# Optimization experiments

Measured on AMD Instinct MI355X. Metric: run time of the kernel, lower is better.

Reference implementation:

```python
import jax, jax.numpy as jnp
import numpy as np

H, D, LORA = 12, 64, 64  # n_heads, headdim, decay-LoRA rank


def _time_mix(x, mu, w_bias, dw1, dw2, u, Wr, Wk, Wv, Wg, Wo, ln_w, ln_b):
    """RWKV-6 time-mix (single direction). x: (B,T,C)."""
    B, T, C = x.shape
    # token shift: previous token (zero-padded at t=0)
    xs = jnp.concatenate([jnp.zeros_like(x[:, :1]), x[:, :-1]], axis=1)
    dx = xs - x
    xr, xk, xv, xw, xg = (x + dx * mu[i] for i in range(5))  # order: r,k,v,w,g
    r = (xr @ Wr).reshape(B, T, H, D)
    k = (xk @ Wk).reshape(B, T, H, D)
    v = (xv @ Wv).reshape(B, T, H, D)
    g = jax.nn.silu(xg @ Wg)                                   # (B,T,C)
    # data-dependent per-channel decay in (0,1)
    w = jnp.exp(-jnp.exp(w_bias + jnp.tanh(xw @ dw1) @ dw2)).reshape(B, T, H, D)

    def step(S, rkvw):  # S: (B,H,D,D) state
        r_t, k_t, v_t, w_t = rkvw          # each (B,H,D)
        kv = k_t[..., None] * v_t[:, :, None, :]               # (B,H,D,D)
        y_t = jnp.einsum('bhd,bhde->bhe', r_t, S + u[None, :, :, None] * kv)
        return w_t[..., None] * S + kv, y_t

    seq = tuple(jnp.moveaxis(a, 1, 0) for a in (r, k, v, w))   # (T,B,H,D)
    S0 = jnp.zeros((B, H, D, D), x.dtype)
    _, ys = jax.lax.scan(step, S0, seq)
    y = jnp.moveaxis(ys, 0, 1)                                 # (B,T,H,D)
    # per-head GroupNorm (n_heads groups over d_model)
    mean = y.mean(-1, keepdims=True)
    var = y.var(-1, keepdims=True)
    y = ((y - mean) * jax.lax.rsqrt(var + 1e-5)).reshape(B, T, C) * ln_w + ln_b
    return (y * g) @ Wo


def reference(x, pad_mask, mu, w_bias, dw1, dw2, u, Wr, Wk, Wv, Wg, Wo, ln_w, ln_b):
    p = lambda i: (mu[i], w_bias[i], dw1[i], dw2[i], u[i], Wr[i], Wk[i], Wv[i],
                   Wg[i], Wo[i], ln_w[i], ln_b[i])
    fwd_out = _time_mix(x, *p(0))
    bwd_out = _time_mix(x[:, ::-1], *p(1))[:, ::-1]
    out = fwd_out + bwd_out
    out = out * pad_mask[..., None].astype(out.dtype)
    return out


def setup_inputs() -> dict:
    key = jax.random.key(0)
    ks = jax.random.split(key, 12)
    B, T, C = 4, 1024, 768
    s = C ** -0.5
    return {
        'x': jax.random.normal(ks[0], (B, T, C), jnp.float32),
        'pad_mask': jnp.ones((B, T), jnp.bool_),
        'mu': jax.random.uniform(ks[1], (2, 5, C), jnp.float32),
        'w_bias': jax.random.normal(ks[2], (2, C), jnp.float32) * 0.3 - 0.5,
        'dw1': jax.random.normal(ks[3], (2, C, LORA), jnp.float32) * s,
        'dw2': jax.random.normal(ks[4], (2, LORA, C), jnp.float32) * 0.1,
        'u': jax.random.normal(ks[5], (2, H, D), jnp.float32) * 0.5,
        'Wr': jax.random.normal(ks[6], (2, C, C), jnp.float32) * s,
        'Wk': jax.random.normal(ks[7], (2, C, C), jnp.float32) * s,
        'Wv': jax.random.normal(ks[8], (2, C, C), jnp.float32) * s,
        'Wg': jax.random.normal(ks[9], (2, C, C), jnp.float32) * s,
        'Wo': jax.random.normal(ks[10], (2, C, C), jnp.float32) * s,
        'ln_w': jnp.ones((2, C), jnp.float32),
        'ln_b': jnp.zeros((2, C), jnp.float32),
    }
```

## Files before the change

kernel.cpp:

```cpp
#include <hip/hip_runtime.h>
#include <cstdint>
#include <cstddef>


#define HH   12
#define DD   64
#define CC   768
#define TT   1024
#define BBB  4
#define LR   64
#define BT   (BBB*TT)
#define WSQ  (CC*CC)

typedef unsigned short u16;
typedef _Float16 f16x8 __attribute__((ext_vector_type(8)));
typedef float f32x4 __attribute__((ext_vector_type(4)));

__device__ __forceinline__ u16 f2h(float f) {
    const _Float16 h = (_Float16)f;
    return __builtin_bit_cast(u16, h);
}
__device__ __forceinline__ float h2f(u16 h) {
    return (float)__builtin_bit_cast(_Float16, h);
}

__device__ __forceinline__ void gl_lds16(const void* g, void* l) {
    __builtin_amdgcn_global_load_lds(
        (const __attribute__((address_space(1))) void*)g,
        (__attribute__((address_space(3))) void*)l, 16, 0, 0);
}

__device__ __forceinline__ float mask_val(const void* mp, int idx) {
    const unsigned char* b = (const unsigned char*)mp;
    const int i0 = ((const int*)mp)[0];
    if (i0 == 0x3f800000) {
        return ((const float*)mp)[idx] != 0.f ? 1.f : 0.f;
    }
    if ((b[1] | b[2] | b[3]) == 0) {
        return ((const int*)mp)[idx] != 0 ? 1.f : 0.f;
    }
    return b[idx] ? 1.f : 0.f;
}

struct TP10 { const float* src[10]; };

__global__ __launch_bounds__(256)
void transpose_conv(TP10 tj, u16* __restrict__ dst)
{
    __shared__ float sh[32][33];
    const int j = blockIdx.z;
    const float* __restrict__ src = tj.src[j];
    u16* __restrict__ d = dst + (size_t)j * WSQ;
    const int n0 = blockIdx.x << 5, k0 = blockIdx.y << 5;
    const int tx = threadIdx.x & 31, ty = threadIdx.x >> 5;
    #pragma unroll
    for (int i = 0; i < 4; ++i)
        sh[ty + (i << 3)][tx] = src[(size_t)(k0 + ty + (i << 3)) * CC + n0 + tx];
    __syncthreads();
    #pragma unroll
    for (int i = 0; i < 4; ++i)
        d[(size_t)(n0 + ty + (i << 3)) * CC + k0 + tx] =
            f2h(sh[tx][ty + (i << 3)]);
}

__global__ __launch_bounds__(256)
void convert_x(const float* __restrict__ x, u16* __restrict__ xb)
{
    const size_t off = ((size_t)blockIdx.x * 256 + threadIdx.x) * 8;
    const float4 a = *reinterpret_cast<const float4*>(x + off);
    const float4 b = *reinterpret_cast<const float4*>(x + off + 4);
    uint4 w;
    w.x = (unsigned)f2h(a.x) | ((unsigned)f2h(a.y) << 16);
    w.y = (unsigned)f2h(a.z) | ((unsigned)f2h(a.w) << 16);
    w.z = (unsigned)f2h(b.x) | ((unsigned)f2h(b.y) << 16);
    w.w = (unsigned)f2h(b.z) | ((unsigned)f2h(b.w) << 16);
    *reinterpret_cast<uint4*>(xb + off) = w;
}

__global__ __launch_bounds__(256)
void convert_mu(const float* __restrict__ mu, u16* __restrict__ muh, int n)
{
    const int i = blockIdx.x * 256 + threadIdx.x;
    if (i < n) muh[i] = f2h(mu[i]);
}

__global__ __launch_bounds__(256)
void mix4_kernel(const u16* __restrict__ xb, const u16* __restrict__ muh,
                 u16* __restrict__ mx, const int dbase)
{
    const int j = blockIdx.y;
    const int slot = blockIdx.z;
    const int dir = dbase + slot;
    const int idx = blockIdx.x * 256 + threadIdx.x;
    const int s = idx / 96;
    const int c = (idx - s * 96) << 3;
    const int b = s >> 10, ts = s & (TT - 1);
    const int t = dir ? (TT - 1 - ts) : ts;
    const int tp = dir ? (t + 1) : (t - 1);
    const int musel = (j == 3) ? 4 : j;

    const uint4 xa4 = *reinterpret_cast<const uint4*>(
        xb + (size_t)(b * TT + t) * CC + c);
    uint4 xp4 = make_uint4(0u, 0u, 0u, 0u);
    if (ts > 0)
        xp4 = *reinterpret_cast<const uint4*>(
            xb + (size_t)(b * TT + tp) * CC + c);
    const uint4 m4 = *reinterpret_cast<const uint4*>(
        muh + (size_t)dir * 5 * CC + musel * CC + c);

    const f16x8 xa = __builtin_bit_cast(f16x8, xa4);
    const f16x8 xp = __builtin_bit_cast(f16x8, xp4);
    const f16x8 mm = __builtin_bit_cast(f16x8, m4);
    const f16x8 res = (xp - xa) * mm + xa;

    u16* __restrict__ dst = mx + (size_t)((slot << 2) + j) * ((size_t)BT * CC);
    *reinterpret_cast<uint4*>(dst + (size_t)s * CC + c) =
        __builtin_bit_cast(uint4, res);
}

struct GB { const u16* Wt[8]; const u16* Ab[8]; float* out[8];
            const float* mu[8]; int act[8]; int dirv[8]; };

__global__ __launch_bounds__(256)
void gemm_mfma_big(GB p, const u16* __restrict__ xb,
                   const int K, const int N, const int mixA)
{
    const int j = blockIdx.z;
    const u16* __restrict__ Wt = p.Wt[j];
    const u16* __restrict__ Ab = p.Ab[j];
    float* __restrict__ out = p.out[j];
    const float* __restrict__ mu = p.mu[j];
    const int act = p.act[j];
    const int dir = p.dirv[j];

    __shared__ __align__(16) u16 Als[128][64];
    __shared__ __align__(16) u16 Bls[128][64];
    const int tid = threadIdx.x;
    const int rowbase = blockIdx.x << 7;
    const int colbase = blockIdx.y << 7;
    const int lane = tid & 63;
    const int wid = tid >> 6;
    const int wr = (wid >> 1) << 6;
    const int wc = (wid & 1) << 6;
    const int lm = lane & 15;

    const int lrow = lane >> 3;
    const int gcol = (((lane & 7) ^ lrow) << 3);

    f32x4 acc[4][4] = {};

    for (int k0 = 0; k0 < K; k0 += 64) {
        if (mixA) {
            #pragma unroll
            for (int it = 0; it < 4; ++it) {
                const int c   = tid + (it << 8);
                const int row = c >> 3;
                const int ch  = c & 7;
                const int kq  = (ch ^ (row & 7)) << 3;
                *reinterpret_cast<uint4*>(&Bls[row][ch << 3]) =
                    *reinterpret_cast<const uint4*>(
                        Wt + (size_t)(colbase + row) * K + k0 + kq);
                const int s  = rowbase + row;
                const int bb = s >> 10, ts = s & (TT - 1);
                const int t  = dir ? (TT - 1 - ts) : ts;
                const int tp = dir ? (t + 1) : (t - 1);
                const uint4 xa4 = *reinterpret_cast<const uint4*>(
                    xb + (size_t)(bb * TT + t) * CC + k0 + kq);
                uint4 xp4 = make_uint4(0u, 0u, 0u, 0u);
                if (ts > 0)
                    xp4 = *reinterpret_cast<const uint4*>(
                        xb + (size_t)(bb * TT + tp) * CC + k0 + kq);
                const u16* as = reinterpret_cast<const u16*>(&xa4);
                const u16* ps = reinterpret_cast<const u16*>(&xp4);
                const float4 m0 = *reinterpret_cast<const float4*>(mu + k0 + kq);
                const float4 m1 = *reinterpret_cast<const float4*>(mu + k0 + kq + 4);
                const float mm[8] = {m0.x, m0.y, m0.z, m0.w,
                                     m1.x, m1.y, m1.z, m1.w};
                uint4 w;
                unsigned rr[4];
                #pragma unroll
                for (int q = 0; q < 4; ++q) {
                    const float a0 = h2f(as[2 * q]);
                    const float a1 = h2f(as[2 * q + 1]);
                    const float p0 = h2f(ps[2 * q]);
                    const float p1 = h2f(ps[2 * q + 1]);
                    const float v0 = fmaf(p0 - a0, mm[2 * q], a0);
                    const float v1 = fmaf(p1 - a1, mm[2 * q + 1], a1);
                    rr[q] = (unsigned)f2h(v0) | ((unsigned)f2h(v1) << 16);
                }
                w.x = rr[0]; w.y = rr[1]; w.z = rr[2]; w.w = rr[3];
                *reinterpret_cast<uint4*>(&Als[row][ch << 3]) = w;
            }
        } else {
            #pragma unroll
            for (int i = 0; i < 4; ++i) {
                const int rb  = (wid << 5) + (i << 3);
                const int row = rb + lrow;
                gl_lds16(Ab + (size_t)(rowbase + row) * K + k0 + gcol,
                         &Als[rb][0]);
                gl_lds16(Wt + (size_t)(colbase + row) * K + k0 + gcol,
                         &Bls[rb][0]);
            }
        }
        __syncthreads();
        #pragma unroll
        for (int ks = 0; ks < 2; ++ks) {
            const int gc = (ks << 2) + (lane >> 4);
            const int sl = (gc ^ (lm & 7)) << 3;
            f16x8 av[4], bv[4];
            #pragma unroll
            for (int mi = 0; mi < 4; ++mi)
                av[mi] = *reinterpret_cast<const f16x8*>(
                    &Als[wr + mi * 16 + lm][sl]);
            #pragma unroll
            for (int ni = 0; ni < 4; ++ni)
                bv[ni] = *reinterpret_cast<const f16x8*>(
                    &Bls[wc + ni * 16 + lm][sl]);
            #pragma unroll
            for (int mi = 0; mi < 4; ++mi)
                #pragma unroll
                for (int ni = 0; ni < 4; ++ni)
                    acc[mi][ni] = __builtin_amdgcn_mfma_f32_16x16x32_f16(
                        av[mi], bv[ni], acc[mi][ni], 0, 0, 0);
        }
        __syncthreads();
    }

    #pragma unroll
    for (int mi = 0; mi < 4; ++mi) {
        #pragma unroll
        for (int r = 0; r < 4; ++r) {
            const int srow = rowbase + wr + mi * 16 + ((lane >> 4) << 2) + r;
            if (act <= 1) {
                #pragma unroll
                for (int ni = 0; ni < 4; ++ni) {
                    float v = acc[mi][ni][r];
                    if (act == 1) v = v / (1.f + expf(-v));
                    out[(size_t)srow * N + colbase + wc + ni * 16 + lm] = v;
                }
            } else {
                const int b2  = srow >> 10;
                const int ts2 = srow & (TT - 1);
                const int t2  = dir ? (TT - 1 - ts2) : ts2;
                float* op = out + (size_t)(b2 * TT + t2) * CC + colbase + wc + lm;
                #pragma unroll
                for (int ni = 0; ni < 4; ++ni)
                    op[ni * 16] = acc[mi][ni][r];
            }
        }
    }
}

__global__ __launch_bounds__(256)
void combine_kernel(float* __restrict__ out, const float* __restrict__ obuf,
                    const void* __restrict__ mask)
{
    const size_t idx = ((size_t)blockIdx.x * 256 + threadIdx.x) * 4;
    const int row = (int)(idx / CC);
    const float mv = mask_val(mask, row);
    const float4 a = *reinterpret_cast<const float4*>(out + idx);
    const float4 b = *reinterpret_cast<const float4*>(obuf + idx);
    *reinterpret_cast<float4*>(out + idx) = make_float4(
        (a.x + b.x) * mv, (a.y + b.y) * mv, (a.z + b.z) * mv, (a.w + b.w) * mv);
}

__global__ __launch_bounds__(256)
void lora1_kernel(const float* __restrict__ x, const float* __restrict__ mu,
                  const float* __restrict__ dw1, float* __restrict__ out,
                  const int dbase)
{
    __shared__ float As[16][68];
    __shared__ float Bs[64][68];
    const int tid = threadIdx.x;
    const int rowbase = blockIdx.x << 4;
    const int slot = blockIdx.y;
    const int dir = dbase + slot;
    const float* __restrict__ muD = mu + (size_t)dir * 5 * CC + 3 * CC;
    const float* __restrict__ dw1p = dw1 + (size_t)dir * CC * LR;
    float* __restrict__ outp = out + (size_t)slot * BT * LR;

    const int arow = tid >> 4;
    const int akq  = (tid & 15) << 2;
    const int s  = rowbase + arow;
    const int bb = s >> 10, ts = s & (TT - 1);
    const int t  = dir ? (TT - 1 - ts) : ts;
    const int tp = dir ? (t + 1) : (t - 1);

    const int c0 = tid & 63;
    const int r4 = tid >> 6;

    float acc[4] = {0.f, 0.f, 0.f, 0.f};

    for (int k0 = 0; k0 < CC; k0 += 64) {
        {
            const int c = k0 + akq;
            const float4 xa = *reinterpret_cast<const float4*>(
                x + (size_t)(bb * TT + t) * CC + c);
            float4 xp = make_float4(0.f, 0.f, 0.f, 0.f);
            if (ts > 0)
                xp = *reinterpret_cast<const float4*>(
                    x + (size_t)(bb * TT + tp) * CC + c);
            const float4 m4 = *reinterpret_cast<const float4*>(muD + c);
            float4 va;
            va.x = fmaf(xp.x - xa.x, m4.x, xa.x);
            va.y = fmaf(xp.y - xa.y, m4.y, xa.y);
            va.z = fmaf(xp.z - xa.z, m4.z, xa.z);
            va.w = fmaf(xp.w - xa.w, m4.w, xa.w);
            *reinterpret_cast<float4*>(&As[arow][akq]) = va;
        }
        #pragma unroll
        for (int it = 0; it < 4; ++it) {
            const int c2 = tid + (it << 8);
            const int brow = c2 >> 4, bcol = (c2 & 15) << 2;
            *reinterpret_cast<float4*>(&Bs[brow][bcol]) =
                *reinterpret_cast<const float4*>(
                    dw1p + (size_t)(k0 + brow) * LR + bcol);
        }
        __syncthreads();
        #pragma unroll
        for (int k4 = 0; k4 < 16; ++k4) {
            float bv[4];
            #pragma unroll
            for (int q = 0; q < 4; ++q) bv[q] = Bs[(k4 << 2) + q][c0];
            #pragma unroll
            for (int i = 0; i < 4; ++i) {
                const float4 a4 = *reinterpret_cast<const float4*>(
                    &As[r4 + (i << 2)][k4 << 2]);
                acc[i] = fmaf(a4.x, bv[0], acc[i]);
                acc[i] = fmaf(a4.y, bv[1], acc[i]);
                acc[i] = fmaf(a4.z, bv[2], acc[i]);
                acc[i] = fmaf(a4.w, bv[3], acc[i]);
            }
        }
        __syncthreads();
    }
    #pragma unroll
    for (int i = 0; i < 4; ++i)
        outp[(size_t)(rowbase + r4 + (i << 2)) * LR + c0] = tanhf(acc[i]);
}

__global__ __launch_bounds__(256)
void gemm_kernel(const float* __restrict__ lora, const float* __restrict__ dw2,
                 const float* __restrict__ wbias, float* __restrict__ wwbuf,
                 const int dbase)
{
    __shared__ float As[16][68];
    __shared__ float Bs[16][68];
    const int tid = threadIdx.x;
    const int rowbase = blockIdx.x << 6;
    const int colbase = blockIdx.y << 6;
    const int slot = blockIdx.z;
    const int dir = dbase + slot;
    const float* __restrict__ Ap = lora + (size_t)slot * BT * LR;
    const float* __restrict__ W  = dw2 + (size_t)dir * LR * CC;
    const float* __restrict__ bias = wbias + (size_t)dir * CC;
    float* __restrict__ out = wwbuf + (size_t)slot * BT * CC;

    const int ty = tid >> 4, tx = tid & 15;
    const int am = tid >> 2;
    const int aq = tid & 3;
    const int s  = rowbase + am;
    const int bk = tid >> 4;
    const int bn = (tid & 15) << 2;

    float acc[4][4];
    #pragma unroll
    for (int i = 0; i < 4; ++i)
        #pragma unroll
        for (int j = 0; j < 4; ++j) acc[i][j] = 0.f;

    for (int k0 = 0; k0 < LR; k0 += 16) {
        const float4 va = *reinterpret_cast<const float4*>(
            Ap + (size_t)s * LR + k0 + (aq << 2));
        const float4 vb = *reinterpret_cast<const float4*>(
            W + (size_t)(k0 + bk) * CC + colbase + bn);
        As[(aq << 2) + 0][am] = va.x;
        As[(aq << 2) + 1][am] = va.y;
        As[(aq << 2) + 2][am] = va.z;
        As[(aq << 2) + 3][am] = va.w;
        *reinterpret_cast<float4*>(&Bs[bk][bn]) = vb;
        __syncthreads();
        #pragma unroll
        for (int kk = 0; kk < 16; ++kk) {
            const float4 a  = *reinterpret_cast<const float4*>(&As[kk][ty << 2]);
            const float4 bv = *reinterpret_cast<const float4*>(&Bs[kk][tx << 2]);
            const float av[4]  = {a.x, a.y, a.z, a.w};
            const float bvv[4] = {bv.x, bv.y, bv.z, bv.w};
            #pragma unroll
            for (int i = 0; i < 4; ++i)
                #pragma unroll
                for (int j = 0; j < 4; ++j)
                    acc[i][j] = fmaf(av[i], bvv[j], acc[i][j]);
        }
        __syncthreads();
    }

    #pragma unroll
    for (int i = 0; i < 4; ++i) {
        const int srow = rowbase + (ty << 2) + i;
        const int ncol = colbase + (tx << 2);
        float v[4];
        #pragma unroll
        for (int j = 0; j < 4; ++j)
            v[j] = expf(-expf(acc[i][j] + bias[ncol + j]));
        *reinterpret_cast<float4*>(out + (size_t)srow * CC + ncol) =
            make_float4(v[0], v[1], v[2], v[3]);
    }
}

template<int L>
__global__ __launch_bounds__(64)
void scanA_kernel(const float* __restrict__ kbuf, const float* __restrict__ vbuf,
                  const float* __restrict__ wbuf,
                  float* __restrict__ SL, float* __restrict__ Pbuf)
{
    constexpr int NCHL = TT / L;
    constexpr size_t SLN = (size_t)NCHL * BBB * HH * DD * DD;
    constexpr size_t PN  = (size_t)NCHL * BBB * HH * DD;
    __shared__ float lk[L * DD], lw[L * DD], lv[L * DD];
    const int c = blockIdx.x, h = blockIdx.y;
    const int b = blockIdx.z & (BBB - 1);
    const int slot = blockIdx.z >> 2;
    const size_t boff = (size_t)slot * BT * CC;
    const int e = threadIdx.x;
    const int rowq = e >> 4;
    const int col  = (e & 15) << 2;

    const size_t gbase = boff + (size_t)(b * TT + c * L) * CC + h * DD;
    #pragma unroll
    for (int r4 = 0; r4 < L / 4; ++r4) {
        const int row = (r4 << 2) + rowq;
        const size_t ga = gbase + (size_t)row * CC + col;
        *reinterpret_cast<float4*>(&lk[row * DD + col]) =
            *reinterpret_cast<const float4*>(kbuf + ga);
        *reinterpret_cast<float4*>(&lw[row * DD + col]) =
            *reinterpret_cast<const float4*>(wbuf + ga);
        *reinterpret_cast<float4*>(&lv[row * DD + col]) =
            *reinterpret_cast<const float4*>(vbuf + ga);
    }
    __syncthreads();

    float S[DD];
    #pragma unroll
    for (int d = 0; d < DD; ++d) S[d] = 0.f;
    float P = 1.f;

    for (int t = 0; t < L; ++t) {
        const float ve = lv[t * DD + e];
        P *= lw[t * DD + e];
        #pragma unroll
        for (int d4 = 0; d4 < 16; ++d4) {
            const float4 k4 = *reinterpret_cast<const float4*>(&lk[t * DD + (d4 << 2)]);
            const float4 w4 = *reinterpret_cast<const float4*>(&lw[t * DD + (d4 << 2)]);
            S[(d4 << 2) + 0] = fmaf(w4.x, S[(d4 << 2) + 0], k4.x * ve);
            S[(d4 << 2) + 1] = fmaf(w4.y, S[(d4 << 2) + 1], k4.y * ve);
            S[(d4 << 2) + 2] = fmaf(w4.z, S[(d4 << 2) + 2], k4.z * ve);
            S[(d4 << 2) + 3] = fmaf(w4.w, S[(d4 << 2) + 3], k4.w * ve);
        }
    }

    float* slotp = SL + (size_t)slot * SLN
                 + (size_t)((c * BBB + b) * HH + h) * DD * DD;
    #pragma unroll
    for (int d = 0; d < DD; ++d) slotp[d * DD + e] = S[d];
    Pbuf[(size_t)slot * PN + (size_t)((c * BBB + b) * HH + h) * DD + e] = P;
}

__global__ __launch_bounds__(64)
void scanB_kernel(float* __restrict__ SL, const float* __restrict__ Pbuf,
                  const int nch)
{
    const int h = blockIdx.x, b = blockIdx.y;
    const int dg = blockIdx.z & 3;
    const int slot = blockIdx.z >> 2;
    const size_t SLN = (size_t)nch * BBB * HH * DD * DD;
    const size_t PN  = (size_t)nch * BBB * HH * DD;
    float* __restrict__ SLs = SL + (size_t)slot * SLN;
    const float* __restrict__ Ps = Pbuf + (size_t)slot * PN;
    const int e = threadIdx.x;
    const size_t doff = (size_t)dg * 16 * DD;

    float S[16];
    #pragma unroll
    for (int i = 0; i < 16; ++i) S[i] = 0.f;

    float sl[16], pp[16];
    {
        const float* s0 = SLs + (size_t)(b * HH + h) * DD * DD + doff;
        const float* p0 = Ps + (size_t)(b * HH + h) * DD + dg * 16;
        #pragma unroll
        for (int i = 0; i < 16; ++i) { sl[i] = s0[i * DD + e]; pp[i] = p0[i]; }
    }
    for (int c = 0; c < nch; ++c) {
        float sl2[16], pp2[16];
        if (c + 1 < nch) {
            const float* s1 = SLs + (size_t)(((c + 1) * BBB + b) * HH + h) * DD * DD + doff;
            const float* p1 = Ps + (size_t)(((c + 1) * BBB + b) * HH + h) * DD + dg * 16;
            #pragma unroll
            for (int i = 0; i < 16; ++i) { sl2[i] = s1[i * DD + e]; pp2[i] = p1[i]; }
        }
        float* sc = SLs + (size_t)((c * BBB + b) * HH + h) * DD * DD + doff;
        #pragma unroll
        for (int i = 0; i < 16; ++i) {
            S[i] = fmaf(pp[i], S[i], sl[i]);
            sc[i * DD + e] = S[i];
        }
        #pragma unroll
        for (int i = 0; i < 16; ++i) { sl[i] = sl2[i]; pp[i] = pp2[i]; }
    }
}

template<int L>
__global__ __launch_bounds__(64)
void scanC_kernel(const float* __restrict__ rbuf, const float* __restrict__ kbuf,
                  const float* __restrict__ vbuf, const float* __restrict__ wbuf,
                  const float* __restrict__ gbuf, const float* __restrict__ SL,
                  const float* __restrict__ u, const float* __restrict__ lnw,
                  const float* __restrict__ lnb, u16* __restrict__ zb,
                  const int dbase)
{
    constexpr int NCHL = TT / L;
    constexpr size_t SLN = (size_t)NCHL * BBB * HH * DD * DD;
    __shared__ float lr[L * DD], lk[L * DD], lw[L * DD];
    const int c = blockIdx.x, h = blockIdx.y;
    const int b = blockIdx.z & (BBB - 1);
    const int slot = blockIdx.z >> 2;
    const int dir = dbase + slot;
    const size_t boff = (size_t)slot * BT * CC;
    const int e = threadIdx.x;
    const int rowq = e >> 4;
    const int col  = (e & 15) << 2;

    const size_t gbase = boff + (size_t)(b * TT + c * L) * CC + h * DD;
    #pragma unroll
    for (int r4 = 0; r4 < L / 4; ++r4) {
        const int row = (r4 << 2) + rowq;
        const size_t ga = gbase + (size_t)row * CC + col;
        *reinterpret_cast<float4*>(&lr[row * DD + col]) =
            *reinterpret_cast<const float4*>(rbuf + ga);
        *reinterpret_cast<float4*>(&lk[row * DD + col]) =
            *reinterpret_cast<const float4*>(kbuf + ga);
        *reinterpret_cast<float4*>(&lw[row * DD + col]) =
            *reinterpret_cast<const float4*>(wbuf + ga);
    }
    __syncthreads();

    const float ue = u[(size_t)(dir * HH + h) * DD + e];
    const float gw = lnw[dir * CC + h * DD + e];
    const float gb = lnb[dir * CC + h * DD + e];

    float S[DD];
    if (c == 0) {
        #pragma unroll
        for (int d = 0; d < DD; ++d) S[d] = 0.f;
    } else {
        const float* slotp = SL + (size_t)slot * SLN
                           + (size_t)(((c - 1) * BBB + b) * HH + h) * DD * DD;
        #pragma unroll
        for (int d = 0; d < DD; ++d) S[d] = slotp[d * DD + e];
    }

    float ve = vbuf[gbase + e];
    float ge = gbuf[gbase + e];
    for (int t = 0; t < L; ++t) {
        float ve2 = 0.f, ge2 = 0.f;
        if (t + 1 < L) {
            ve2 = vbuf[gbase + (size_t)(t + 1) * CC + e];
            ge2 = gbuf[gbase + (size_t)(t + 1) * CC + e];
        }
        float coef = lr[t * DD + e] * ue * lk[t * DD + e];
        #pragma unroll
        for (int off = 32; off > 0; off >>= 1) coef += __shfl_xor(coef, off);

        float y0 = 0.f, y1 = 0.f, y2 = 0.f, y3 = 0.f;
        #pragma unroll
        for (int d4 = 0; d4 < 16; ++d4) {
            const float4 r4 = *reinterpret_cast<const float4*>(&lr[t * DD + (d4 << 2)]);
            const float4 k4 = *reinterpret_cast<const float4*>(&lk[t * DD + (d4 << 2)]);
            const float4 w4 = *reinterpret_cast<const float4*>(&lw[t * DD + (d4 << 2)]);
            y0 = fmaf(r4.x, S[(d4 << 2) + 0], y0);
            y1 = fmaf(r4.y, S[(d4 << 2) + 1], y1);
            y2 = fmaf(r4.z, S[(d4 << 2) + 2], y2);
            y3 = fmaf(r4.w, S[(d4 << 2) + 3], y3);
            S[(d4 << 2) + 0] = fmaf(w4.x, S[(d4 << 2) + 0], k4.x * ve);
            S[(d4 << 2) + 1] = fmaf(w4.y, S[(d4 << 2) + 1], k4.y * ve);
            S[(d4 << 2) + 2] = fmaf(w4.z, S[(d4 << 2) + 2], k4.z * ve);
            S[(d4 << 2) + 3] = fmaf(w4.w, S[(d4 << 2) + 3], k4.w * ve);
        }
        float y = ((y0 + y1) + (y2 + y3)) + coef * ve;

        float sum = y, sq = y * y;
        #pragma unroll
        for (int off = 32; off > 0; off >>= 1) {
            sum += __shfl_xor(sum, off);
            sq  += __shfl_xor(sq, off);
        }
        const float mean = sum * (1.f / 64.f);
        const float var  = fmaf(-mean, mean, sq * (1.f / 64.f));
        const float yn   = (y - mean) * rsqrtf(var + 1e-5f) * gw + gb;
        zb[gbase + (size_t)t * CC + e] = f2h(yn * ge);
        ve = ve2;
        ge = ge2;
    }
}

extern "C" void kernel_launch(void* const* d_in, const int* in_sizes, int n_in,
                              void* d_out, int out_size, void* d_ws, size_t ws_size,
                              hipStream_t stream)
{
    const float* x     = (const float*)d_in[0];
    const void*  mask  = d_in[1];
    const float* mu    = (const float*)d_in[2];
    const float* wbias = (const float*)d_in[3];
    const float* dw1   = (const float*)d_in[4];
    const float* dw2   = (const float*)d_in[5];
    const float* u     = (const float*)d_in[6];
    const float* Wr    = (const float*)d_in[7];
    const float* Wk    = (const float*)d_in[8];
    const float* Wv    = (const float*)d_in[9];
    const float* Wg    = (const float*)d_in[10];
    const float* Wo    = (const float*)d_in[11];
    const float* lnw   = (const float*)d_in[12];
    const float* lnb   = (const float*)d_in[13];
    float* out = (float*)d_out;

    float* ws = (float*)d_ws;
    const size_t NBT = (size_t)BT * CC;
    const size_t MUN = 2 * 5 * CC;

    auto fits = [&](int nd, int nch, bool mb) -> bool {
        const size_t SLN = (size_t)nch * BBB * HH * DD * DD;
        const size_t PN  = (size_t)nch * BBB * HH * DD;
        const size_t fl = (size_t)nd * (5 * NBT + (size_t)BT * LR + SLN + PN);
        const size_t hw = (size_t)(nd + 1) * NBT + (size_t)10 * WSQ + MUN
                        + (mb ? (size_t)4 * nd * NBT : 0);
        return fl * 4 + hw * 2 <= ws_size;
    };
    int nd, nch; bool mixbuf;
    if      (fits(2, 64, true)) { nd = 2; nch = 64; mixbuf = true; }
    else if (fits(2, 32, true)) { nd = 2; nch = 32; mixbuf = true; }
    else if (fits(2, 16, true)) { nd = 2; nch = 16; mixbuf = true; }
    else {
        nd = 1;
        mixbuf = fits(1, 16, true);
        nch = fits(1, 64, mixbuf) ? 64 : fits(1, 32, mixbuf) ? 32 : 16;
    }
    const size_t SLN = (size_t)nch * BBB * HH * DD * DD;
    const size_t PN  = (size_t)nch * BBB * HH * DD;

    float* rbuf  = ws;
    float* kbuf  = rbuf  + (size_t)nd * NBT;
    float* vbuf  = kbuf  + (size_t)nd * NBT;
    float* wwbuf = vbuf  + (size_t)nd * NBT;
    float* gbuf  = wwbuf + (size_t)nd * NBT;
    float* lora  = gbuf  + (size_t)nd * NBT;
    float* SL    = lora  + (size_t)nd * BT * LR;
    float* Pbuf  = SL    + (size_t)nd * SLN;
    u16*   zb    = (u16*)(Pbuf + (size_t)nd * PN);
    u16*   xbb   = zb + (size_t)nd * NBT;
    u16*   wtb   = xbb + NBT;
    u16*   muh   = wtb + (size_t)10 * WSQ;
    u16*   mx    = muh + MUN;
    float* obuf  = rbuf;

    TP10 tj;
    const float* Wlist[5] = {Wr, Wk, Wv, Wg, Wo};
    for (int dir = 0; dir < 2; ++dir)
        for (int i = 0; i < 5; ++i)
            tj.src[dir * 5 + i] = Wlist[i] + (size_t)dir * WSQ;
    transpose_conv<<<dim3(24, 24, 10), 256, 0, stream>>>(tj, wtb);
    convert_x<<<dim3((int)(NBT / (8 * 256))), 256, 0, stream>>>(x, xbb);
    convert_mu<<<dim3((int)((MUN + 255) / 256)), 256, 0, stream>>>(mu, muh, (int)MUN);

    auto launch_scans = [&](int ndl, int dbase) {
        const dim3 zA(TT / (TT / nch), 1, 1);
        if (nch == 64) {
            scanA_kernel<16><<<dim3(64, HH, BBB * ndl), dim3(64), 0, stream>>>(
                kbuf, vbuf, wwbuf, SL, Pbuf);
            scanB_kernel<<<dim3(HH, BBB, 4 * ndl), dim3(64), 0, stream>>>(SL, Pbuf, 64);
            scanC_kernel<16><<<dim3(64, HH, BBB * ndl), dim3(64), 0, stream>>>(
                rbuf, kbuf, vbuf, wwbuf, gbuf, SL, u, lnw, lnb, zb, dbase);
        } else if (nch == 32) {
            scanA_kernel<32><<<dim3(32, HH, BBB * ndl), dim3(64), 0, stream>>>(
                kbuf, vbuf, wwbuf, SL, Pbuf);
            scanB_kernel<<<dim3(HH, BBB, 4 * ndl), dim3(64), 0, stream>>>(SL, Pbuf, 32);
            scanC_kernel<32><<<dim3(32, HH, BBB * ndl), dim3(64), 0, stream>>>(
                rbuf, kbuf, vbuf, wwbuf, gbuf, SL, u, lnw, lnb, zb, dbase);
        } else {
            scanA_kernel<64><<<dim3(16, HH, BBB * ndl), dim3(64), 0, stream>>>(
                kbuf, vbuf, wwbuf, SL, Pbuf);
            scanB_kernel<<<dim3(HH, BBB, 4 * ndl), dim3(64), 0, stream>>>(SL, Pbuf, 16);
            scanC_kernel<64><<<dim3(16, HH, BBB * ndl), dim3(64), 0, stream>>>(
                rbuf, kbuf, vbuf, wwbuf, gbuf, SL, u, lnw, lnb, zb, dbase);
        }
    };

    if (nd == 2) {
        mix4_kernel<<<dim3((int)(NBT / (8 * 256)), 4, 2), 256, 0, stream>>>(
            xbb, muh, mx, 0);

        GB pb;
        float* outs[4] = {rbuf, kbuf, vbuf, gbuf};
        for (int s = 0; s < 2; ++s) {
            const u16* wt = wtb + (size_t)s * 5 * WSQ;
            for (int j = 0; j < 4; ++j) {
                const int jj = s * 4 + j;
                pb.Wt[jj]  = wt + (size_t)j * WSQ;
                pb.Ab[jj]  = mx + (size_t)jj * NBT;
                pb.out[jj] = outs[j] + (size_t)s * NBT;
                pb.mu[jj]  = mu;
                pb.act[jj] = (j == 3) ? 1 : 0;
                pb.dirv[jj] = s;
            }
        }
        gemm_mfma_big<<<dim3(BT / 128, CC / 128, 8), 256, 0, stream>>>(
            pb, xbb, CC, CC, 0);

        lora1_kernel<<<dim3(BT / 16, 2), 256, 0, stream>>>(x, mu, dw1, lora, 0);
        gemm_kernel<<<dim3(BT / 64, CC / 64, 2), 256, 0, stream>>>(
            lora, dw2, wbias, wwbuf, 0);

        launch_scans(2, 0);

        GB po = {};
        for (int s = 0; s < 2; ++s) {
            po.Wt[s]  = wtb + (size_t)s * 5 * WSQ + (size_t)4 * WSQ;
            po.Ab[s]  = zb + (size_t)s * NBT;
            po.out[s] = (s == 0) ? out : obuf;
            po.mu[s]  = mu;
            po.act[s] = 4;
            po.dirv[s] = s;
        }
        gemm_mfma_big<<<dim3(BT / 128, CC / 128, 2), 256, 0, stream>>>(
            po, xbb, CC, CC, 0);
    } else {
        for (int d = 0; d < 2; ++d) {
            const u16* wt = wtb + (size_t)d * 5 * WSQ;
            GB pb;
            float* outs[4] = {rbuf, kbuf, vbuf, gbuf};
            for (int j = 0; j < 4; ++j) {
                pb.Wt[j]  = wt + (size_t)j * WSQ;
                pb.Ab[j]  = mx + (size_t)j * NBT;
                pb.out[j] = outs[j];
                pb.mu[j]  = mu + (size_t)d * 5 * CC + (size_t)((j == 3) ? 4 : j) * CC;
                pb.act[j] = (j == 3) ? 1 : 0;
                pb.dirv[j] = d;
            }
            if (mixbuf) {
                mix4_kernel<<<dim3((int)(NBT / (8 * 256)), 4, 1), 256, 0, stream>>>(
                    xbb, muh, mx, d);
                gemm_mfma_big<<<dim3(BT / 128, CC / 128, 4), 256, 0, stream>>>(
                    pb, xbb, CC, CC, 0);
            } else {
                gemm_mfma_big<<<dim3(BT / 128, CC / 128, 4), 256, 0, stream>>>(
                    pb, xbb, CC, CC, 1);
            }
            lora1_kernel<<<dim3(BT / 16, 1), 256, 0, stream>>>(x, mu, dw1, lora, d);
            gemm_kernel<<<dim3(BT / 64, CC / 64, 1), 256, 0, stream>>>(
                lora, dw2, wbias, wwbuf, d);

            launch_scans(1, d);

            GB po = {};
            po.Wt[0]  = wt + (size_t)4 * WSQ;
            po.Ab[0]  = zb;
            po.out[0] = (d == 0) ? out : obuf;
            po.mu[0]  = mu;
            po.act[0] = 4;
            po.dirv[0] = d;
            gemm_mfma_big<<<dim3(BT / 128, CC / 128, 1), 256, 0, stream>>>(
                po, xbb, CC, CC, 0);
        }
    }

    combine_kernel<<<dim3((int)(NBT / (4 * 256))), 256, 0, stream>>>(
        out, obuf, mask);
}
```

Measured before the change: 353.3 us.

## Rewrite chunk scan output kernel with fp16-packed r/k and fused GroupNorm reduction

Replaces the templated scanC kernel with a version that stores r and k as packed fp16 pairs in shared memory, keeps the running state in registers, and computes the per-token intra-chunk output and u-bonus term in one pass. It then does a shuffle-based GroupNorm reduction across the head dimension in shared memory before gating and writing fp16 output. The L=64 path keeps the old kernel, renamed scanC_old. The aim is to cut shared-memory footprint and bandwidth and to fuse the normalization. In exchange, r and k lose precision by going through fp16.

Measured after the change: 389.1 us. 1.1x slower.

```diff
diff --git a/kernel.cpp b/kernel.cpp
--- a/kernel.cpp
+++ b/kernel.cpp
@@ -521,6 +521,142 @@
 {
     constexpr int NCHL = TT / L;
     constexpr size_t SLN = (size_t)NCHL * BBB * HH * DD * DD;
+    __shared__ unsigned lrk[L * DD];
+    __shared__ float lw[L * DD];
+    __shared__ float ys[L * 65], pcs[L * 65], vs[L * 65];
+    __shared__ float redm[L], redi[L];
+
+    const int c = blockIdx.x, h = blockIdx.y;
+    const int b = blockIdx.z & (BBB - 1);
+    const int slot = blockIdx.z >> 2;
+    const int dir = dbase + slot;
+    const size_t boff = (size_t)slot * BT * CC;
+    const int e = threadIdx.x;
+    const int rowq = e >> 4;
+    const int col  = (e & 15) << 2;
+
+    const size_t gbase = boff + (size_t)(b * TT + c * L) * CC + h * DD;
+    #pragma unroll
+    for (int r4 = 0; r4 < L / 4; ++r4) {
+        const int row = (r4 << 2) + rowq;
+        const size_t ga = gbase + (size_t)row * CC + col;
+        const float4 rv = *reinterpret_cast<const float4*>(rbuf + ga);
+        const float4 kv = *reinterpret_cast<const float4*>(kbuf + ga);
+        const float4 wv = *reinterpret_cast<const float4*>(wbuf + ga);
+        *reinterpret_cast<float4*>(&lw[row * DD + col]) = wv;
+        uint4 pk;
+        pk.x = (unsigned)f2h(rv.x) | ((unsigned)f2h(kv.x) << 16);
+        pk.y = (unsigned)f2h(rv.y) | ((unsigned)f2h(kv.y) << 16);
+        pk.z = (unsigned)f2h(rv.z) | ((unsigned)f2h(kv.z) << 16);
+        pk.w = (unsigned)f2h(rv.w) | ((unsigned)f2h(kv.w) << 16);
+        *reinterpret_cast<uint4*>(&lrk[row * DD + col]) = pk;
+    }
+    __syncthreads();
+
+    const float ue = u[(size_t)(dir * HH + h) * DD + e];
+    const float gw = lnw[dir * CC + h * DD + e];
+    const float gb = lnb[dir * CC + h * DD + e];
+
+    float S[DD];
+    if (c == 0) {
+        #pragma unroll
+        for (int d = 0; d < DD; ++d) S[d] = 0.f;
+    } else {
+        const float* slotp = SL + (size_t)slot * SLN
+                           + (size_t)(((c - 1) * BBB + b) * HH + h) * DD * DD;
+        #pragma unroll
+        for (int d = 0; d < DD; ++d) S[d] = slotp[d * DD + e];
+    }
+
+    float ve = vbuf[gbase + e];
+    float re = rbuf[gbase + e];
+    float ke = kbuf[gbase + e];
+    for (int t = 0; t < L; ++t) {
+        float ve2 = 0.f, re2 = 0.f, ke2 = 0.f;
+        if (t + 1 < L) {
+            ve2 = vbuf[gbase + (size_t)(t + 1) * CC + e];
+            re2 = rbuf[gbase + (size_t)(t + 1) * CC + e];
+            ke2 = kbuf[gbase + (size_t)(t + 1) * CC + e];
+        }
+        float y0 = 0.f, y1 = 0.f, y2 = 0.f, y3 = 0.f;
+        #pragma unroll
+        for (int d4 = 0; d4 < 16; ++d4) {
+            const uint4 rk4 = *reinterpret_cast<const uint4*>(
+                &lrk[t * DD + (d4 << 2)]);
+            const float4 w4 = *reinterpret_cast<const float4*>(
+                &lw[t * DD + (d4 << 2)]);
+            const float r0 = h2f((u16)(rk4.x & 0xffffu)), k0 = h2f((u16)(rk4.x >> 16));
+            const float r1 = h2f((u16)(rk4.y & 0xffffu)), k1 = h2f((u16)(rk4.y >> 16));
+            const float r2 = h2f((u16)(rk4.z & 0xffffu)), k2 = h2f((u16)(rk4.z >> 16));
+            const float r3 = h2f((u16)(rk4.w & 0xffffu)), k3 = h2f((u16)(rk4.w >> 16));
+            y0 = fmaf(r0, S[(d4 << 2) + 0], y0);
+            y1 = fmaf(r1, S[(d4 << 2) + 1], y1);
+            y2 = fmaf(r2, S[(d4 << 2) + 2], y2);
+            y3 = fmaf(r3, S[(d4 << 2) + 3], y3);
+            S[(d4 << 2) + 0] = fmaf(w4.x, S[(d4 << 2) + 0], k0 * ve);
+            S[(d4 << 2) + 1] = fmaf(w4.y, S[(d4 << 2) + 1], k1 * ve);
+            S[(d4 << 2) + 2] = fmaf(w4.z, S[(d4 << 2) + 2], k2 * ve);
+            S[(d4 << 2) + 3] = fmaf(w4.w, S[(d4 << 2) + 3], k3 * ve);
+        }
+        ys[t * 65 + e]  = (y0 + y1) + (y2 + y3);
+        pcs[t * 65 + e] = re * ue * ke;
+        vs[t * 65 + e]  = ve;
+        ve = ve2; re = re2; ke = ke2;
+    }
+    __syncthreads();
+
+    constexpr int HPT = 64 / L;
+    constexpr int SEG = 64 / HPT;
+    {
+        const int t1 = e / HPT;
+        const int h1 = e % HPT;
+        const int off0 = t1 * 65 + h1 * SEG;
+        float cp = 0.f;
+        #pragma unroll
+        for (int jq = 0; jq < SEG; ++jq) cp += pcs[off0 + jq];
+        #pragma unroll
+        for (int off = 1; off < HPT; off <<= 1) cp += __shfl_xor(cp, off);
+        float sm = 0.f, sq = 0.f;
+        #pragma unroll
+        for (int jq = 0; jq < SEG; ++jq) {
+            const float yf = fmaf(cp, vs[off0 + jq], ys[off0 + jq]);
+            ys[off0 + jq] = yf;
+            sm += yf;
+            sq = fmaf(yf, yf, sq);
+        }
+        #pragma unroll
+        for (int off = 1; off < HPT; off <<= 1) {
+            sm += __shfl_xor(sm, off);
+            sq += __shfl_xor(sq, off);
+        }
+        if (h1 == 0) {
+            const float mean = sm * (1.f / 64.f);
+            const float var  = fmaf(-mean, mean, sq * (1.f / 64.f));
+            redm[t1] = mean;
+            redi[t1] = rsqrtf(var + 1e-5f);
+        }
+    }
+    __syncthreads();
+
+    for (int t = 0; t < L; ++t) {
+        const float yf = ys[t * 65 + e];
+        const float yn = (yf - redm[t]) * redi[t] * gw + gb;
+        zb[gbase + (size_t)t * CC + e] =
+            f2h(yn * gbuf[gbase + (size_t)t * CC + e]);
+    }
+}
+
+__global__ __launch_bounds__(64)
+void scanC_old(const float* __restrict__ rbuf, const float* __restrict__ kbuf,
+               const float* __restrict__ vbuf, const float* __restrict__ wbuf,
+               const float* __restrict__ gbuf, const float* __restrict__ SL,
+               const float* __restrict__ u, const float* __restrict__ lnw,
+               const float* __restrict__ lnb, u16* __restrict__ zb,
+               const int dbase)
+{
+    constexpr int L = 64;
+    constexpr int NCHL = TT / L;
+    constexpr size_t SLN = (size_t)NCHL * BBB * HH * DD * DD;
     __shared__ float lr[L * DD], lk[L * DD], lw[L * DD];
     const int c = blockIdx.x, h = blockIdx.y;
     const int b = blockIdx.z & (BBB - 1);
@@ -673,7 +809,6 @@
     convert_mu<<<dim3((int)((MUN + 255) / 256)), 256, 0, stream>>>(mu, muh, (int)MUN);
 
     auto launch_scans = [&](int ndl, int dbase) {
-        const dim3 zA(TT / (TT / nch), 1, 1);
         if (nch == 64) {
             scanA_kernel<16><<<dim3(64, HH, BBB * ndl), dim3(64), 0, stream>>>(
                 kbuf, vbuf, wwbuf, SL, Pbuf);
@@ -690,7 +825,7 @@
             scanA_kernel<64><<<dim3(16, HH, BBB * ndl), dim3(64), 0, stream>>>(
                 kbuf, vbuf, wwbuf, SL, Pbuf);
             scanB_kernel<<<dim3(HH, BBB, 4 * ndl), dim3(64), 0, stream>>>(SL, Pbuf, 16);
-            scanC_kernel<64><<<dim3(16, HH, BBB * ndl), dim3(64), 0, stream>>>(
+            scanC_old<<<dim3(16, HH, BBB * ndl), dim3(64), 0, stream>>>(
                 rbuf, kbuf, vbuf, wwbuf, gbuf, SL, u, lnw, lnb, zb, dbase);
         }
     };
```
